# Performance work log

Hardware: AMD Instinct MI355X
Metric: run time of the kernel (lower is better)

Reference implementation:

```python
import jax, jax.numpy as jnp
import numpy as np
from math import floor, log2

DEPTH = 4
DIM = 1024
HEADS = 16
DIM_HEAD = 64
FF_MULT = 4
NUM_TOKENS = 32000
SEQ = 2048
MASK_VALUE = -1e10
EPS = 1e-5
ATTN_INNER = DIM_HEAD * HEADS            # 1024
FF_INNER = DIM * FF_MULT                 # 4096
FUSED = (ATTN_INNER, DIM_HEAD, DIM_HEAD, FF_INNER, FF_INNER)  # q, k, v, ff, ff_gate


def get_alibi_slopes(heads):
    def pow2_slopes(n):
        start = 2 ** (-2 ** (-(log2(n) - 3)))
        return [start * start ** i for i in range(n)]
    if log2(heads).is_integer():
        return pow2_slopes(heads)
    c = 2 ** floor(log2(heads))
    return pow2_slopes(c) + pow2_slopes(2 * c)[0::2][: heads - c]


def make_attn_bias(seq_len, heads, mask_value):
    # ALiBi variant used by this module: bias depends only on key position j
    slopes = np.array(get_alibi_slopes(heads), dtype=np.float32)[:, None, None]  # [h,1,1]
    bias = slopes * np.arange(seq_len, dtype=np.float32)[None, None, :]          # [h,1,j]
    bias = np.broadcast_to(bias, (heads, seq_len, seq_len))
    causal = np.tril(np.ones((seq_len, seq_len), dtype=bool))
    return jnp.asarray(np.where(causal, bias, mask_value), dtype=jnp.float32)


def rmsnorm(x, gamma):
    ssq = jnp.sum(jnp.square(x), axis=-1, keepdims=True)
    return jax.lax.rsqrt(ssq + EPS) * x * gamma * (x.shape[-1] ** 0.5)


def block(x, attn_bias, wi, attn_wo, ff_wo, gamma):
    h = rmsnorm(x, gamma)
    splits = np.cumsum(FUSED[:-1])
    q, k, v, ff, ff_gate = jnp.split(h @ wi, splits, axis=-1)
    b, n, _ = q.shape
    # multi-query attention: k, v have a single shared head of size DIM_HEAD
    q = q.reshape(b, n, HEADS, DIM_HEAD).transpose(0, 2, 1, 3) * (DIM_HEAD ** -0.5)
    sim = jnp.einsum('bhid,bjd->bhij', q, k) + attn_bias
    attn = jax.nn.softmax(sim, axis=-1)
    out = jnp.einsum('bhij,bjd->bhid', attn, v)
    out = out.transpose(0, 2, 1, 3).reshape(b, n, ATTN_INNER)
    attn_out = out @ attn_wo
    ff_out = (ff * jax.nn.swish(ff_gate)) @ ff_wo
    return attn_out + ff_out


def setup_inputs() -> dict:
    key = jax.random.key(0)
    ks = jax.random.split(key, 6)
    return {
        'tokens': jax.random.randint(ks[0], (1, SEQ), 0, NUM_TOKENS),
        'embedding': jax.random.normal(ks[1], (NUM_TOKENS, DIM), jnp.float32) * 0.02,
        'wi': jax.random.normal(ks[2], (DEPTH, DIM, sum(FUSED)), jnp.float32),
        'attn_wo': jax.random.normal(ks[3], (DEPTH, ATTN_INNER, DIM), jnp.float32),
        'ff_wo': jax.random.normal(ks[4], (DEPTH, FF_INNER, DIM), jnp.float32),
        'gammas': jnp.ones((DEPTH, DIM), jnp.float32),
        'final_gamma': jnp.ones((DIM,), jnp.float32),
    }


def reference(tokens, embedding, wi, attn_wo, ff_wo, gammas, final_gamma):
    n = tokens.shape[-1]
    attn_bias = make_attn_bias(SEQ, HEADS, MASK_VALUE)[..., :n, :n]
    x = embedding[tokens]                     # [b, n, dim]
    for l in range(DEPTH):
        x = block(x, attn_bias, wi[l], attn_wo[l], ff_wo[l], gammas[l]) + x
    x = rmsnorm(x, final_gamma)
    return x @ embedding.T                    # tied-embedding logits [b, n, vocab]
```

## Files before the change

### kernel.cpp

```cpp
#include <hip/hip_runtime.h>
#include <stdint.h>


typedef __attribute__((ext_vector_type(8))) __bf16 bf16x8;
typedef __attribute__((ext_vector_type(4))) __bf16 bf16x4;
typedef __attribute__((ext_vector_type(8))) short s16x8;
typedef __attribute__((ext_vector_type(4))) float f32x4;

#define SEQ   2048
#define DIM   1024
#define NHEAD 16
#define DHEAD 64
#define FUSEN 9344
#define QKW   1088
#define FFIN  4096
#define VOCAB 32000
#define AFW   5120
#define LOG2E 1.44269504f

__device__ __forceinline__ f32x4 mfma16(bf16x8 a, bf16x8 b, f32x4 c) {
  return __builtin_amdgcn_mfma_f32_16x16x32_bf16(
      __builtin_bit_cast(s16x8, a), __builtin_bit_cast(s16x8, b), c, 0, 0, 0);
}

__device__ __forceinline__ void load_lds16(const __bf16* g, __bf16* l) {
  __builtin_amdgcn_global_load_lds(
      (const __attribute__((address_space(1))) uint32_t*)g,
      (__attribute__((address_space(3))) uint32_t*)l, 16, 0, 0);
}


__global__ void cast_k(const float* __restrict__ in, __bf16* __restrict__ out, int n8) {
  int i = blockIdx.x * 256 + threadIdx.x;
  if (i >= n8) return;
  const float4* p = (const float4*)in + (size_t)i * 2;
  float4 a = p[0], b = p[1];
  bf16x8 o;
  o[0] = (__bf16)a.x; o[1] = (__bf16)a.y; o[2] = (__bf16)a.z; o[3] = (__bf16)a.w;
  o[4] = (__bf16)b.x; o[5] = (__bf16)b.y; o[6] = (__bf16)b.z; o[7] = (__bf16)b.w;
  *(bf16x8*)(out + (size_t)i * 8) = o;
}

__global__ void gather_k(const int* __restrict__ tokens, const float* __restrict__ emb,
                         float* __restrict__ x) {
  int n = blockIdx.x;
  int tok = tokens[n];
  float4 v = ((const float4*)(emb + (size_t)tok * DIM))[threadIdx.x];
  ((float4*)(x + (size_t)n * DIM))[threadIdx.x] = v;
}

__device__ __forceinline__ int permcol(int c) {
  if (c < 1152) return c;
  if (c < 5248) { int i = c - 1152; return 1152 + ((i >> 4) << 5) + (i & 15); }
  int i = c - 5248; return 1152 + ((i >> 4) << 5) + 16 + (i & 15);
}

__global__ __launch_bounds__(256) void transpose_wi_k(
    const float* __restrict__ in, __bf16* __restrict__ out) {
  __shared__ float tile[32][33];
  int l = blockIdx.z;
  int tx = threadIdx.x & 31, ty = threadIdx.x >> 5;
  int c0 = blockIdx.x * 32, r0 = blockIdx.y * 32;
  const float* inl = in + (size_t)l * DIM * FUSEN;
  __bf16* outl = out + (size_t)l * FUSEN * DIM;
  for (int i = ty; i < 32; i += 8)
    tile[i][tx] = inl[(size_t)(r0 + i) * FUSEN + c0 + tx];
  __syncthreads();
  for (int i = ty; i < 32; i += 8)
    outl[(size_t)permcol(c0 + i) * DIM + r0 + tx] = (__bf16)tile[tx][i];
}

__global__ __launch_bounds__(256) void transpose_b_k(
    const float* __restrict__ in, __bf16* __restrict__ out,
    int R, int C, int ldo, int co, size_t outLstride) {
  __shared__ float tile[32][33];
  int l = blockIdx.z;
  int tx = threadIdx.x & 31, ty = threadIdx.x >> 5;
  int c0 = blockIdx.x * 32, r0 = blockIdx.y * 32;
  const float* inl = in + (size_t)l * R * C;
  __bf16* outl = out + (size_t)l * outLstride;
  for (int i = ty; i < 32; i += 8)
    tile[i][tx] = inl[(size_t)(r0 + i) * C + c0 + tx];
  __syncthreads();
  for (int i = ty; i < 32; i += 8)
    outl[(size_t)(c0 + i) * ldo + co + r0 + tx] = (__bf16)tile[tx][i];
}

template <int HASP>
__global__ __launch_bounds__(256) void rmsnorm_fuse_k(
    const float* __restrict__ x, const float* __restrict__ p,
    const float* __restrict__ gamma, float* __restrict__ xn,
    __bf16* __restrict__ h) {
  int n = blockIdx.x;
  float4 v = ((const float4*)(x + (size_t)n * DIM))[threadIdx.x];
  if (HASP) {
    float4 a = ((const float4*)(p + (size_t)n * DIM))[threadIdx.x];
    float4 b = ((const float4*)(p + (size_t)(SEQ + n) * DIM))[threadIdx.x];
    v.x += a.x + b.x; v.y += a.y + b.y; v.z += a.z + b.z; v.w += a.w + b.w;
    ((float4*)(xn + (size_t)n * DIM))[threadIdx.x] = v;
  }
  float ssq = v.x * v.x + v.y * v.y + v.z * v.z + v.w * v.w;
  for (int m = 32; m >= 1; m >>= 1) ssq += __shfl_xor(ssq, m, 64);
  __shared__ float red[4];
  if ((threadIdx.x & 63) == 0) red[threadIdx.x >> 6] = ssq;
  __syncthreads();
  float tot = red[0] + red[1] + red[2] + red[3];
  float rs = rsqrtf(tot + 1e-5f) * 32.0f;
  float4 g = ((const float4*)gamma)[threadIdx.x];
  bf16x4 o;
  o[0] = (__bf16)(v.x * rs * g.x);
  o[1] = (__bf16)(v.y * rs * g.y);
  o[2] = (__bf16)(v.z * rs * g.z);
  o[3] = (__bf16)(v.w * rs * g.w);
  *(bf16x4*)(h + (size_t)n * DIM + threadIdx.x * 4) = o;
}

template <int MODE>
__global__ __launch_bounds__(256) void gemm_bt_k(
    const __bf16* __restrict__ A, int lda,
    const __bf16* __restrict__ Bt, int ldb,
    float* __restrict__ outf, int ldc,
    __bf16* __restrict__ qh, __bf16* __restrict__ ql,
    __bf16* __restrict__ vT, __bf16* __restrict__ aof,
    int K) {
  __shared__ __bf16 lA[8192];
  __shared__ __bf16 lB[8192];
  const int t = threadIdx.x;
  const int lane = t & 63, wave = t >> 6;
  const int lo4 = lane & 15, hi2 = lane >> 4;
  const int nwg = gridDim.x * gridDim.y;
  const int orig = blockIdx.y * gridDim.x + blockIdx.x;
  const int xcd = orig & 7, off = orig >> 3;
  const int qq = nwg >> 3, rr = nwg & 7;
  const int nid = (xcd < rr ? xcd * (qq + 1) : rr * (qq + 1) + (xcd - rr) * qq) + off;
  const int bm = nid % gridDim.y, bn = nid / gridDim.y;
  const int k0 = blockIdx.z * K;
  const int wr = (wave >> 1) * 64, wc = (wave & 1) * 64;

  f32x4 acc[4][4];
#pragma unroll
  for (int m = 0; m < 4; m++)
#pragma unroll
    for (int n = 0; n < 4; n++) acc[m][n] = f32x4{0.f, 0.f, 0.f, 0.f};

  const int e0 = t * 8;
  const int e1 = 2048 + t * 8;
  const __bf16* gA0 = A + (size_t)(bm * 128 + (e0 >> 5)) * lda + (e0 & 31) + k0;
  const __bf16* gA1 = A + (size_t)(bm * 128 + (e1 >> 5)) * lda + (e1 & 31) + k0;
  const __bf16* gB0 = Bt + (size_t)(bn * 128 + (e0 >> 5)) * ldb + (e0 & 31) + k0;
  const __bf16* gB1 = Bt + (size_t)(bn * 128 + (e1 >> 5)) * ldb + (e1 & 31) + k0;
  __bf16* dA0 = &lA[wave * 512];
  __bf16* dA1 = &lA[2048 + wave * 512];
  __bf16* dB0 = &lB[wave * 512];
  __bf16* dB1 = &lB[2048 + wave * 512];

  for (int kt = 0; kt < K; kt += 64) {
    load_lds16(gA0 + kt, dA0);
    load_lds16(gA1 + kt, dA1);
    load_lds16(gB0 + kt, dB0);
    load_lds16(gB1 + kt, dB1);
    load_lds16(gA0 + kt + 32, dA0 + 4096);
    load_lds16(gA1 + kt + 32, dA1 + 4096);
    load_lds16(gB0 + kt + 32, dB0 + 4096);
    load_lds16(gB1 + kt + 32, dB1 + 4096);
    __syncthreads();
#pragma unroll
    for (int half = 0; half < 2; half++) {
      const __bf16* sA = &lA[half * 4096];
      const __bf16* sB = &lB[half * 4096];
      bf16x8 af[4], bf_[4];
#pragma unroll
      for (int m = 0; m < 4; m++)
        af[m] = *(const bf16x8*)&sA[(wr + m * 16 + lo4) * 32 + hi2 * 8];
#pragma unroll
      for (int n = 0; n < 4; n++)
        bf_[n] = *(const bf16x8*)&sB[(wc + n * 16 + lo4) * 32 + hi2 * 8];
#pragma unroll
      for (int m = 0; m < 4; m++)
#pragma unroll
        for (int n = 0; n < 4; n++)
          acc[m][n] = mfma16(af[m], bf_[n], acc[m][n]);
    }
    __syncthreads();
  }

  if (MODE == 0) {
    float* op = outf + (size_t)blockIdx.z * SEQ * DIM;
#pragma unroll
    for (int m = 0; m < 4; m++) {
      const int rowb = bm * 128 + wr + m * 16 + hi2 * 4;
#pragma unroll
      for (int n = 0; n < 4; n++) {
        const int col = bn * 128 + wc + n * 16 + lo4;
#pragma unroll
        for (int j = 0; j < 4; j++)
          __builtin_nontemporal_store(acc[m][n][j], &op[(size_t)(rowb + j) * ldc + col]);
      }
    }
  } else if (bn < 8 || (bn == 8 && wc == 0)) {
#pragma unroll
    for (int m = 0; m < 4; m++) {
      const int rowb = bm * 128 + wr + m * 16 + hi2 * 4;
#pragma unroll
      for (int n = 0; n < 4; n++) {
        const int col = bn * 128 + wc + n * 16 + lo4;
#pragma unroll
        for (int j = 0; j < 4; j++) {
          float v = acc[m][n][j];
          __bf16 hi = (__bf16)v;
          qh[(size_t)(rowb + j) * QKW + col] = hi;
          ql[(size_t)(rowb + j) * QKW + col] = (__bf16)(v - (float)hi);
        }
      }
    }
  } else if (bn == 8) {
#pragma unroll
    for (int m = 0; m < 4; m++) {
      const int rowb = bm * 128 + wr + m * 16 + hi2 * 4;
#pragma unroll
      for (int n = 0; n < 4; n++) {
        const int vcol = n * 16 + lo4;
#pragma unroll
        for (int j = 0; j < 4; j++)
          vT[(size_t)vcol * SEQ + rowb + j] = (__bf16)acc[m][n][j];
      }
    }
  } else {
#pragma unroll
    for (int m = 0; m < 4; m++) {
      const int rowb = bm * 128 + wr + m * 16 + hi2 * 4;
#pragma unroll
      for (int np = 0; np < 4; np += 2) {
        const int cb = (bn - 9) * 128 + wc + np * 16;
        const int acol = 1024 + ((cb >> 5) << 4) + lo4;
#pragma unroll
        for (int j = 0; j < 4; j++) {
          float ff = acc[m][np][j];
          float gg = acc[m][np + 1][j];
          float s = gg / (1.f + expf(-gg));
          aof[(size_t)(rowb + j) * AFW + acol] = (__bf16)(ff * s);
        }
      }
    }
  }
}

__global__ __launch_bounds__(512, 1) void gemm256_k(
    const __bf16* __restrict__ A, const __bf16* __restrict__ Bt,
    float* __restrict__ C, int ldc, int K) {
  __shared__ __bf16 lds[65536];
  const int t = threadIdx.x;
  const int lane = t & 63, w = t >> 6;
  const int lo4 = lane & 15, hi2 = lane >> 4;
  const int wr = w >> 2, wc = w & 3;
  const int nwg = gridDim.x * gridDim.y;
  const int orig = blockIdx.y * gridDim.x + blockIdx.x;
  const int xcd = orig & 7, off = orig >> 3;
  const int qq = nwg >> 3, rr = nwg & 7;
  const int nid = (xcd < rr ? xcd * (qq + 1) : rr * (qq + 1) + (xcd - rr) * qq) + off;
  const int bm = nid % gridDim.y, bn = nid / gridDim.y;

  const int srow = lane >> 2;
  const int scol = ((lane & 3) * 8) ^ ((lane >> 5) << 4);
  const __bf16* gA = A + (size_t)(bm * 256 + srow) * K + scol;
  const __bf16* gB = Bt + (size_t)(bn * 256 + srow) * K + scol;
  const int cpr = (hi2 * 8) ^ ((lo4 >= 8) ? 16 : 0);

  auto STAGE = [&](int kt, int ks, int isB) {
    const __bf16* g = (isB ? gB : gA) + kt * 64 + ks * 32;
    __bf16* l = &lds[isB * 32768 + (kt & 1) * 16384 + ks * 8192 + (2 * w) * 512];
    load_lds16(g + (size_t)(2 * w) * 16 * K, l);
    load_lds16(g + (size_t)(2 * w + 1) * 16 * K, l + 512);
  };

  f32x4 acc[8][4];
#pragma unroll
  for (int m = 0; m < 8; m++)
#pragma unroll
    for (int n = 0; n < 4; n++) acc[m][n] = f32x4{0.f, 0.f, 0.f, 0.f};

  STAGE(0, 0, 0); STAGE(0, 0, 1); STAGE(0, 1, 0); STAGE(0, 1, 1);

  const int NIT = K >> 7;
  bf16x8 bfr[4];
  for (int it = 0; it < NIT; ++it) {
#pragma unroll
    for (int p = 0; p < 8; ++p) {
      const int g = p >> 2;
      const int u = p & 3;
      const int ks = u >> 1, mh = u & 1;
      const int kt = 2 * it + g;
      const bool dostage = (it < NIT - 1) || (g == 0);
      if ((u & 1) == 0) {
        if (it == NIT - 1 && g == 1 && u == 2)
          asm volatile("s_waitcnt vmcnt(0)" ::: "memory");
        else
          asm volatile("s_waitcnt vmcnt(4)" ::: "memory");
        __builtin_amdgcn_s_barrier();
      }
      const int abase = g * 16384 + ks * 8192 + lo4 * 32 + cpr;
      if ((u & 1) == 0) {
#pragma unroll
        for (int n = 0; n < 4; n++)
          bfr[n] = *(const bf16x8*)&lds[32768 + abase + (wc * 4 + n) * 512];
      }
      bf16x8 af[4];
#pragma unroll
      for (int mm = 0; mm < 4; mm++)
        af[mm] = *(const bf16x8*)&lds[abase + (wr * 8 + mh * 4 + mm) * 512];
      if (dostage) STAGE(kt + 1, ks, u & 1);
      __builtin_amdgcn_s_setprio(1);
#pragma unroll
      for (int mm = 0; mm < 4; mm++)
#pragma unroll
        for (int n = 0; n < 4; n++)
          acc[mh * 4 + mm][n] = mfma16(af[mm], bfr[n], acc[mh * 4 + mm][n]);
      __builtin_amdgcn_s_setprio(0);
    }
  }

#pragma unroll
  for (int m = 0; m < 8; m++) {
    const int rowb = bm * 256 + wr * 128 + m * 16 + hi2 * 4;
#pragma unroll
    for (int n = 0; n < 4; n++) {
      const int col = bn * 256 + wc * 64 + n * 16 + lo4;
#pragma unroll
      for (int j = 0; j < 4; j++)
        __builtin_nontemporal_store(acc[m][n][j], &C[(size_t)(rowb + j) * ldc + col]);
    }
  }
}

__global__ __launch_bounds__(256, 4) void flash_k(
    const __bf16* __restrict__ qh, const __bf16* __restrict__ ql,
    const __bf16* __restrict__ vT, __bf16* __restrict__ aof) {
  const int t = threadIdx.x;
  const int lane = t & 63, wave = t >> 6;
  const int lo4 = lane & 15, hi2 = lane >> 4;
  const int b = blockIdx.x;
  const int h = b & 15;
  const int s = b >> 4;
  const int pr = wave >> 1, half = wave & 1;
  const int c = pr ? (127 - s) : s;
  const int qrow0 = c * 16;
  const int nt = (c >> 2) + 1;
  const int ntA = (nt + 1) >> 1;
  const int jt0 = half ? ntA : 0;
  const int jtE = half ? nt : ntA;
  const float slope2 = exp2f(-0.5f * (float)(h + 1)) * LOG2E;
  const float scale2 = 0.125f * LOG2E;

  __shared__ __bf16 lP[4][16][72];
  __shared__ float smO[2][2][16][65];
  __shared__ float sml[2][2][16][2];
  __bf16 (*lPw)[72] = lP[wave];

  bf16x8 qhf[2], qlf[2];
#pragma unroll
  for (int kk = 0; kk < 2; kk++) {
    size_t qoff = (size_t)(qrow0 + lo4) * QKW + h * 64 + kk * 32 + hi2 * 8;
    qhf[kk] = *(const bf16x8*)(qh + qoff);
    qlf[kk] = *(const bf16x8*)(ql + qoff);
  }

  float jb[4][4];
#pragma unroll
  for (int f = 0; f < 4; f++)
#pragma unroll
    for (int r = 0; r < 4; r++)
      jb[f][r] = slope2 * (float)(jt0 * 64 + f * 16 + hi2 * 4 + r);
  const float dj = slope2 * 64.0f;
  const int iq = qrow0 + lo4;

  f32x4 O[4];
#pragma unroll
  for (int f = 0; f < 4; f++) O[f] = f32x4{0.f, 0.f, 0.f, 0.f};
  float mr = -1e30f, lr = 0.f;

  for (int jt = jt0; jt < jtE; ++jt) {
    f32x4 sc[4];
#pragma unroll
    for (int f = 0; f < 4; f++) sc[f] = f32x4{0.f, 0.f, 0.f, 0.f};
    __builtin_amdgcn_s_setprio(1);
#pragma unroll
    for (int kk = 0; kk < 2; kk++) {
#pragma unroll
      for (int f = 0; f < 4; f++) {
        size_t koff = (size_t)(jt * 64 + f * 16 + lo4) * QKW + 1024 + kk * 32 + hi2 * 8;
        bf16x8 khf = *(const bf16x8*)(qh + koff);
        bf16x8 klf = *(const bf16x8*)(ql + koff);
        sc[f] = mfma16(khf, qlf[kk], sc[f]);
        sc[f] = mfma16(klf, qhf[kk], sc[f]);
        sc[f] = mfma16(khf, qhf[kk], sc[f]);
      }
    }
    __builtin_amdgcn_s_setprio(0);

    float pv[4][4];
    float tmax = -1e30f;
#pragma unroll
    for (int f = 0; f < 4; f++)
#pragma unroll
      for (int r = 0; r < 4; r++) {
        const int j = jt * 64 + f * 16 + hi2 * 4 + r;
        float v = fmaf(sc[f][r], scale2, jb[f][r]);
        if (j > iq) v = -1e30f;
        pv[f][r] = v;
        tmax = fmaxf(tmax, v);
      }
    tmax = fmaxf(tmax, __shfl_xor(tmax, 16, 64));
    tmax = fmaxf(tmax, __shfl_xor(tmax, 32, 64));
    float mn = fmaxf(mr, tmax);
    float corr = exp2f(mr - mn);
    mr = mn;
    float rs = 0.f;
#pragma unroll
    for (int f = 0; f < 4; f++)
#pragma unroll
      for (int r = 0; r < 4; r++) {
        float pe = exp2f(pv[f][r] - mn);
        __bf16 pb = (__bf16)pe;
        lPw[lo4][f * 16 + hi2 * 4 + r] = pb;
        rs += (float)pb;
      }
    rs += __shfl_xor(rs, 16, 64);
    rs += __shfl_xor(rs, 32, 64);
    lr = lr * corr + rs;
    float co[4];
#pragma unroll
    for (int r = 0; r < 4; r++)
      co[r] = __shfl(corr, (lane & 48) + hi2 * 4 + r, 64);
#pragma unroll
    for (int f = 0; f < 4; f++)
#pragma unroll
      for (int r = 0; r < 4; r++) O[f][r] *= co[r];

    __builtin_amdgcn_s_setprio(1);
#pragma unroll
    for (int kk = 0; kk < 2; kk++) {
      bf16x8 pa = *(const bf16x8*)&lPw[lo4][kk * 32 + hi2 * 8];
#pragma unroll
      for (int f = 0; f < 4; f++) {
        bf16x8 vb = *(const bf16x8*)(vT + (size_t)(f * 16 + lo4) * SEQ + jt * 64 + kk * 32 + hi2 * 8);
        O[f] = mfma16(pa, vb, O[f]);
      }
    }
    __builtin_amdgcn_s_setprio(0);

#pragma unroll
    for (int f = 0; f < 4; f++)
#pragma unroll
      for (int r = 0; r < 4; r++) jb[f][r] += dj;
  }

#pragma unroll
  for (int f = 0; f < 4; f++)
#pragma unroll
    for (int r = 0; r < 4; r++)
      smO[pr][half][hi2 * 4 + r][f * 16 + lo4] = O[f][r];
  if (hi2 == 0) {
    sml[pr][half][lo4][0] = mr;
    sml[pr][half][lo4][1] = lr;
  }
  __syncthreads();
  if (half == 0) {
#pragma unroll
    for (int r = 0; r < 4; r++) {
      const int row = hi2 * 4 + r;
      float mA = sml[pr][0][row][0], lA = sml[pr][0][row][1];
      float mB = sml[pr][1][row][0], lB = sml[pr][1][row][1];
      float mS = fmaxf(mA, mB);
      float cA = exp2f(mA - mS), cB = exp2f(mB - mS);
      float li = lA * cA + lB * cB;
#pragma unroll
      for (int f = 0; f < 4; f++) {
        float v = (smO[pr][0][row][f * 16 + lo4] * cA +
                   smO[pr][1][row][f * 16 + lo4] * cB) / li;
        aof[(size_t)(qrow0 + row) * AFW + h * 64 + f * 16 + lo4] = (__bf16)v;
      }
    }
  }
}


extern "C" void kernel_launch(void* const* d_in, const int* in_sizes, int n_in,
                              void* d_out, int out_size, void* d_ws, size_t ws_size,
                              hipStream_t stream) {
  const int* tokens  = (const int*)d_in[0];
  const float* emb   = (const float*)d_in[1];
  const float* wi    = (const float*)d_in[2];
  const float* awo   = (const float*)d_in[3];
  const float* fwo   = (const float*)d_in[4];
  const float* gam   = (const float*)d_in[5];
  const float* fgam  = (const float*)d_in[6];
  float* out = (float*)d_out;

  char* wsp = (char*)d_ws;
  size_t woff = 0;
  auto walloc = [&](size_t b) { void* p = wsp + woff; woff += (b + 255) & ~(size_t)255; return p; };
  __bf16* embb = (__bf16*)walloc((size_t)VOCAB * DIM * 2);
  __bf16* h    = (__bf16*)walloc((size_t)SEQ * DIM * 2);

  char* op = (char*)d_out;
  size_t ooff = 0;
  auto oalloc = [&](size_t b) { void* p = op + ooff; ooff += (b + 255) & ~(size_t)255; return p; };
  float*  xA    = (float*)oalloc((size_t)SEQ * DIM * 4);
  float*  xB    = (float*)oalloc((size_t)SEQ * DIM * 4);
  float*  pp    = (float*)oalloc((size_t)2 * SEQ * DIM * 4);
  __bf16* qhb   = (__bf16*)oalloc((size_t)SEQ * QKW * 2);
  __bf16* qlb   = (__bf16*)oalloc((size_t)SEQ * QKW * 2);
  __bf16* vT    = (__bf16*)oalloc((size_t)DHEAD * SEQ * 2);
  __bf16* aof   = (__bf16*)oalloc((size_t)SEQ * AFW * 2);
  __bf16* wiT4  = (__bf16*)oalloc((size_t)4 * FUSEN * DIM * 2);
  __bf16* BT24  = (__bf16*)oalloc((size_t)4 * DIM * AFW * 2);
  (void)ws_size; (void)in_sizes; (void)n_in; (void)out_size;

  cast_k<<<(VOCAB * DIM / 8 + 255) / 256, 256, 0, stream>>>(emb, embb, VOCAB * DIM / 8);
  gather_k<<<SEQ, 256, 0, stream>>>(tokens, emb, xA);
  transpose_wi_k<<<dim3(FUSEN / 32, DIM / 32, 4), 256, 0, stream>>>(wi, wiT4);
  transpose_b_k<<<dim3(DIM / 32, DIM / 32, 4), 256, 0, stream>>>(
      awo, BT24, DIM, DIM, AFW, 0, (size_t)DIM * AFW);
  transpose_b_k<<<dim3(DIM / 32, FFIN / 32, 4), 256, 0, stream>>>(
      fwo, BT24, FFIN, DIM, AFW, 1024, (size_t)DIM * AFW);

  float* x = xA;
  float* xn = xB;
  for (int l = 0; l < 4; l++) {
    if (l == 0) {
      rmsnorm_fuse_k<0><<<SEQ, 256, 0, stream>>>(x, nullptr, gam, nullptr, h);
    } else {
      rmsnorm_fuse_k<1><<<SEQ, 256, 0, stream>>>(x, pp, gam + l * DIM, xn, h);
      float* tmp = x; x = xn; xn = tmp;
    }
    gemm_bt_k<1><<<dim3(FUSEN / 128, SEQ / 128), 256, 0, stream>>>(
        h, DIM, wiT4 + (size_t)l * FUSEN * DIM, DIM, nullptr, 0,
        qhb, qlb, vT, aof, DIM);
    flash_k<<<dim3(1024), 256, 0, stream>>>(qhb, qlb, vT, aof);
    gemm_bt_k<0><<<dim3(DIM / 128, SEQ / 128, 2), 256, 0, stream>>>(
        aof, AFW, BT24 + (size_t)l * DIM * AFW, AFW, pp, DIM,
        nullptr, nullptr, nullptr, nullptr, AFW / 2);
  }

  rmsnorm_fuse_k<1><<<SEQ, 256, 0, stream>>>(x, pp, fgam, xn, h);
  gemm256_k<<<dim3(VOCAB / 256, SEQ / 256), 512, 0, stream>>>(
      h, embb, out, VOCAB, DIM);
}
```

Before: 1.219 ms.

## Split flash attention KV range across four waves per query tile; fuse gather into rmsnorm

The flash kernel now gives each block a single 16-row query tile and splits its key range across all four waves, instead of pairing a short and a long tile and splitting each across two waves. The grid doubles to 2048 blocks, and all four waves share the final merge, with vectorized bf16x4 stores. Masked scores are explicitly zeroed, which keeps the result correct when a wave's chunk is entirely masked. Separately, the embedding gather is fused into the first rmsnorm launch, removing one kernel and one pass over the activations; the cost is less work per block and a heavier four-way merge.

```diff
diff --git a/kernel.cpp b/kernel.cpp
--- a/kernel.cpp
+++ b/kernel.cpp
@@ -39,14 +39,6 @@
   o[0] = (__bf16)a.x; o[1] = (__bf16)a.y; o[2] = (__bf16)a.z; o[3] = (__bf16)a.w;
   o[4] = (__bf16)b.x; o[5] = (__bf16)b.y; o[6] = (__bf16)b.z; o[7] = (__bf16)b.w;
   *(bf16x8*)(out + (size_t)i * 8) = o;
-}
-
-__global__ void gather_k(const int* __restrict__ tokens, const float* __restrict__ emb,
-                         float* __restrict__ x) {
-  int n = blockIdx.x;
-  int tok = tokens[n];
-  float4 v = ((const float4*)(emb + (size_t)tok * DIM))[threadIdx.x];
-  ((float4*)(x + (size_t)n * DIM))[threadIdx.x] = v;
 }
 
 __device__ __forceinline__ int permcol(int c) {
@@ -86,14 +78,20 @@
     outl[(size_t)(c0 + i) * ldo + co + r0 + tx] = (__bf16)tile[tx][i];
 }
 
-template <int HASP>
+template <int MODE>
 __global__ __launch_bounds__(256) void rmsnorm_fuse_k(
     const float* __restrict__ x, const float* __restrict__ p,
+    const int* __restrict__ tokens, const float* __restrict__ emb,
     const float* __restrict__ gamma, float* __restrict__ xn,
     __bf16* __restrict__ h) {
   int n = blockIdx.x;
-  float4 v = ((const float4*)(x + (size_t)n * DIM))[threadIdx.x];
-  if (HASP) {
+  float4 v;
+  if (MODE == 0) {
+    int tok = tokens[n];
+    v = ((const float4*)(emb + (size_t)tok * DIM))[threadIdx.x];
+    ((float4*)(xn + (size_t)n * DIM))[threadIdx.x] = v;
+  } else {
+    v = ((const float4*)(x + (size_t)n * DIM))[threadIdx.x];
     float4 a = ((const float4*)(p + (size_t)n * DIM))[threadIdx.x];
     float4 b = ((const float4*)(p + (size_t)(SEQ + n) * DIM))[threadIdx.x];
     v.x += a.x + b.x; v.y += a.y + b.y; v.z += a.z + b.z; v.w += a.w + b.w;
@@ -340,20 +338,18 @@
   const int lo4 = lane & 15, hi2 = lane >> 4;
   const int b = blockIdx.x;
   const int h = b & 15;
-  const int s = b >> 4;
-  const int pr = wave >> 1, half = wave & 1;
-  const int c = pr ? (127 - s) : s;
+  const int c = b >> 4;
   const int qrow0 = c * 16;
   const int nt = (c >> 2) + 1;
-  const int ntA = (nt + 1) >> 1;
-  const int jt0 = half ? ntA : 0;
-  const int jtE = half ? nt : ntA;
+  const int base = nt >> 2, rem = nt & 3;
+  const int jt0 = wave * base + (wave < rem ? wave : rem);
+  const int jtE = jt0 + base + (wave < rem ? 1 : 0);
   const float slope2 = exp2f(-0.5f * (float)(h + 1)) * LOG2E;
   const float scale2 = 0.125f * LOG2E;
 
   __shared__ __bf16 lP[4][16][72];
-  __shared__ float smO[2][2][16][65];
-  __shared__ float sml[2][2][16][2];
+  __shared__ float smO[4][16][68];
+  __shared__ float sml[4][16][2];
   __bf16 (*lPw)[72] = lP[wave];
 
   bf16x8 qhf[2], qlf[2];
@@ -419,7 +415,7 @@
     for (int f = 0; f < 4; f++)
 #pragma unroll
       for (int r = 0; r < 4; r++) {
-        float pe = exp2f(pv[f][r] - mn);
+        float pe = (pv[f][r] > -1e29f) ? exp2f(pv[f][r] - mn) : 0.f;
         __bf16 pb = (__bf16)pe;
         lPw[lo4][f * 16 + hi2 * 4 + r] = pb;
         rs += (float)pb;
@@ -458,28 +454,30 @@
   for (int f = 0; f < 4; f++)
 #pragma unroll
     for (int r = 0; r < 4; r++)
-      smO[pr][half][hi2 * 4 + r][f * 16 + lo4] = O[f][r];
+      smO[wave][hi2 * 4 + r][f * 16 + lo4] = O[f][r];
   if (hi2 == 0) {
-    sml[pr][half][lo4][0] = mr;
-    sml[pr][half][lo4][1] = lr;
+    sml[wave][lo4][0] = mr;
+    sml[wave][lo4][1] = lr;
   }
   __syncthreads();
-  if (half == 0) {
-#pragma unroll
-    for (int r = 0; r < 4; r++) {
-      const int row = hi2 * 4 + r;
-      float mA = sml[pr][0][row][0], lA = sml[pr][0][row][1];
-      float mB = sml[pr][1][row][0], lB = sml[pr][1][row][1];
-      float mS = fmaxf(mA, mB);
-      float cA = exp2f(mA - mS), cB = exp2f(mB - mS);
-      float li = lA * cA + lB * cB;
-#pragma unroll
-      for (int f = 0; f < 4; f++) {
-        float v = (smO[pr][0][row][f * 16 + lo4] * cA +
-                   smO[pr][1][row][f * 16 + lo4] * cB) / li;
-        aof[(size_t)(qrow0 + row) * AFW + h * 64 + f * 16 + lo4] = (__bf16)v;
-      }
-    }
+  {
+    const int row = wave * 4 + hi2;
+    float m0 = sml[0][row][0], m1 = sml[1][row][0];
+    float m2 = sml[2][row][0], m3 = sml[3][row][0];
+    float mS = fmaxf(fmaxf(m0, m1), fmaxf(m2, m3));
+    float c0 = exp2f(m0 - mS), c1 = exp2f(m1 - mS);
+    float c2 = exp2f(m2 - mS), c3 = exp2f(m3 - mS);
+    float li = sml[0][row][1] * c0 + sml[1][row][1] * c1 +
+               sml[2][row][1] * c2 + sml[3][row][1] * c3;
+    bf16x4 o4;
+#pragma unroll
+    for (int cc = 0; cc < 4; cc++) {
+      const int col = lo4 * 4 + cc;
+      float v = (smO[0][row][col] * c0 + smO[1][row][col] * c1 +
+                 smO[2][row][col] * c2 + smO[3][row][col] * c3) / li;
+      o4[cc] = (__bf16)v;
+    }
+    *(bf16x4*)(aof + (size_t)(qrow0 + row) * AFW + h * 64 + lo4 * 4) = o4;
   }
 }
 
@@ -517,7 +515,6 @@
   (void)ws_size; (void)in_sizes; (void)n_in; (void)out_size;
 
   cast_k<<<(VOCAB * DIM / 8 + 255) / 256, 256, 0, stream>>>(emb, embb, VOCAB * DIM / 8);
-  gather_k<<<SEQ, 256, 0, stream>>>(tokens, emb, xA);
   transpose_wi_k<<<dim3(FUSEN / 32, DIM / 32, 4), 256, 0, stream>>>(wi, wiT4);
   transpose_b_k<<<dim3(DIM / 32, DIM / 32, 4), 256, 0, stream>>>(
       awo, BT24, DIM, DIM, AFW, 0, (size_t)DIM * AFW);
@@ -528,21 +525,24 @@
   float* xn = xB;
   for (int l = 0; l < 4; l++) {
     if (l == 0) {
-      rmsnorm_fuse_k<0><<<SEQ, 256, 0, stream>>>(x, nullptr, gam, nullptr, h);
+      rmsnorm_fuse_k<0><<<SEQ, 256, 0, stream>>>(
+          nullptr, nullptr, tokens, emb, gam, x, h);
     } else {
-      rmsnorm_fuse_k<1><<<SEQ, 256, 0, stream>>>(x, pp, gam + l * DIM, xn, h);
+      rmsnorm_fuse_k<1><<<SEQ, 256, 0, stream>>>(
+          x, pp, nullptr, nullptr, gam + l * DIM, xn, h);
       float* tmp = x; x = xn; xn = tmp;
     }
     gemm_bt_k<1><<<dim3(FUSEN / 128, SEQ / 128), 256, 0, stream>>>(
         h, DIM, wiT4 + (size_t)l * FUSEN * DIM, DIM, nullptr, 0,
         qhb, qlb, vT, aof, DIM);
-    flash_k<<<dim3(1024), 256, 0, stream>>>(qhb, qlb, vT, aof);
+    flash_k<<<dim3(2048), 256, 0, stream>>>(qhb, qlb, vT, aof);
     gemm_bt_k<0><<<dim3(DIM / 128, SEQ / 128, 2), 256, 0, stream>>>(
         aof, AFW, BT24 + (size_t)l * DIM * AFW, AFW, pp, DIM,
         nullptr, nullptr, nullptr, nullptr, AFW / 2);
   }
 
-  rmsnorm_fuse_k<1><<<SEQ, 256, 0, stream>>>(x, pp, fgam, xn, h);
+  rmsnorm_fuse_k<1><<<SEQ, 256, 0, stream>>>(
+      x, pp, nullptr, nullptr, fgam, xn, h);
   gemm256_k<<<dim3(VOCAB / 256, SEQ / 256), 512, 0, stream>>>(
       h, embb, out, VOCAB, DIM);
 }
```

New measurement: 1.235 ms. About the same (+1.3%).
